# Optimization experiments

Measured on AMD Instinct MI355X. Metric: run time of the kernel, lower is better.

The kernel has to match this reference:

```python
import jax, jax.numpy as jnp
import numpy as np
import math

D_MODEL = 1024
N_HEADS = 16
HEAD_DIM = 64
BATCH = 2
SEQ = 2048


def setup_inputs() -> dict:
    key = jax.random.key(0)
    ks = jax.random.split(key, 5)
    x = jax.random.normal(ks[0], (BATCH, SEQ, D_MODEL), dtype=jnp.float32)
    s = 0.02
    wq = jax.random.normal(ks[1], (D_MODEL, D_MODEL), dtype=jnp.float32) * s
    wk = jax.random.normal(ks[2], (D_MODEL, D_MODEL), dtype=jnp.float32) * s
    wv = jax.random.normal(ks[3], (D_MODEL, D_MODEL), dtype=jnp.float32) * s
    wo = jax.random.normal(ks[4], (D_MODEL, D_MODEL), dtype=jnp.float32) * s
    gammas = jnp.linspace(0.9, 0.99, N_HEADS, dtype=jnp.float32)
    return {"x": x, "wq": wq, "wk": wk, "wv": wv, "wo": wo, "gammas": gammas}


def _decay_mask(length: int, gammas: jnp.ndarray, dtype) -> jnp.ndarray:
    # [H, L, L]: gamma^(t-s) for t >= s, else 0 (causal exponential decay)
    pos = jnp.arange(length)
    diff = pos[:, None] - pos[None, :]
    causal = diff >= 0
    d = jnp.maximum(diff, 0).astype(dtype)
    g = gammas.astype(dtype)[:, None, None]
    return jnp.where(causal[None], jnp.power(g, d[None]), jnp.zeros((), dtype))


def reference(x, wq, wk, wv, wo, gammas):
    B, L, D = x.shape
    H, hd = N_HEADS, HEAD_DIM
    # torch nn.Linear: y = x @ W.T
    q = (x @ wq.T).reshape(B, L, H, hd)
    k = (x @ wk.T).reshape(B, L, H, hd)
    v = (x @ wv.T).reshape(B, L, H, hd)
    scale = 1.0 / math.sqrt(hd)
    scores = jnp.einsum('bthd,bshd->bhts', q * scale, k)  # [B,H,L,L]
    decay = _decay_mask(L, gammas, x.dtype)               # [H,L,L]
    weights = scores * decay[None]
    retained = jnp.einsum('bhts,bshd->bthd', weights, v)  # [B,L,H,hd]
    return retained.reshape(B, L, H * hd) @ wo.T
```

## Files before the change

kernel.cpp:

```cpp
#include <hip/hip_runtime.h>


typedef __attribute__((ext_vector_type(8))) short bf16x8;
typedef __attribute__((ext_vector_type(4))) float f32x4;
typedef __attribute__((ext_vector_type(16))) float f32x16;
typedef __attribute__((ext_vector_type(4))) unsigned short u16x4;
typedef __attribute__((ext_vector_type(8))) unsigned short u16x8;
typedef __attribute__((ext_vector_type(4))) unsigned int u32x4;

__device__ inline unsigned short f2bf(float f) {
    unsigned int u;
    __builtin_memcpy(&u, &f, 4);
    u += 0x7fffu + ((u >> 16) & 1u);
    return (unsigned short)(u >> 16);
}

__device__ inline f32x4 mfma16(bf16x8 a, bf16x8 b, f32x4 c) {
    return __builtin_amdgcn_mfma_f32_16x16x32_bf16(a, b, c, 0, 0, 0);
}
__device__ inline f32x16 mfma32(bf16x8 a, bf16x8 b, f32x16 c) {
    return __builtin_amdgcn_mfma_f32_32x32x16_bf16(a, b, c, 0, 0, 0);
}

__device__ inline void gl16(const unsigned short* g, unsigned short* l) {
    __builtin_amdgcn_global_load_lds(
        (const __attribute__((address_space(1))) unsigned int*)g,
        (__attribute__((address_space(3))) unsigned int*)l,
        16, 0, 0);
}

__device__ inline unsigned cvtpk(float lo, float hi) {
    unsigned r;
    asm("v_cvt_pk_bf16_f32 %0, %1, %2" : "=v"(r) : "v"(lo), "v"(hi));
    return r;
}

__global__ __launch_bounds__(256) void convert_bf16(
    const float* __restrict__ x,
    const float* __restrict__ wq, const float* __restrict__ wk,
    const float* __restrict__ wv, const float* __restrict__ wo,
    unsigned short* __restrict__ xb,
    unsigned short* __restrict__ wqb, unsigned short* __restrict__ wkb,
    unsigned short* __restrict__ wvb, unsigned short* __restrict__ wob)
{
    int cid = blockIdx.x * 256 + threadIdx.x;
    #pragma unroll
    for (int it = 0; it < 4; ++it, cid += 262144) {
        const float* src;
        unsigned short* dst;
        size_t off;
        if (cid < 524288) {
            src = x; dst = xb; off = (size_t)cid * 8;
        } else {
            const int t = cid - 524288;
            const int seg = t >> 17;
            off = (size_t)(t & 131071) * 8;
            src = seg == 0 ? wq : seg == 1 ? wk : seg == 2 ? wv : wo;
            dst = seg == 0 ? wqb : seg == 1 ? wkb : seg == 2 ? wvb : wob;
        }
        f32x4 a = *(const f32x4*)(src + off);
        f32x4 b = *(const f32x4*)(src + off + 4);
        u32x4 v = { cvtpk(a[0], a[1]), cvtpk(a[2], a[3]),
                    cvtpk(b[0], b[1]), cvtpk(b[2], b[3]) };
        *(u32x4*)(dst + off) = v;
    }
}

__global__ __launch_bounds__(256) void qkv_bf16(
    const unsigned short* __restrict__ xb,
    const unsigned short* __restrict__ wqb, const unsigned short* __restrict__ wkb,
    const unsigned short* __restrict__ wvb,
    unsigned short* __restrict__ qfr, unsigned short* __restrict__ kfr,
    unsigned short* __restrict__ vfr)
{
    __shared__ unsigned short sR[128 * 64];
    __shared__ unsigned short sL[128 * 64];

    const int z = blockIdx.z;
    const unsigned short* W = (z == 0) ? wqb : (z == 1) ? wkb : wvb;
    const unsigned short* Rs = (z < 2) ? xb : W;
    const unsigned short* Ls = (z < 2) ? W : xb;
    const int rblk = (z < 2) ? blockIdx.x : blockIdx.y;
    const int lblk = (z < 2) ? blockIdx.y : blockIdx.x;

    const int tid = threadIdx.x;
    const int l = tid & 63, w = tid >> 6;
    const int lrow = l & 15, koff4 = (l >> 4) * 4;
    const int swz = lrow & 7;
    const int wrow = (w >> 1) * 64, wcol = (w & 1) * 64;

    f32x4 acc[4][4] = {};

    const int srow = w * 32 + (l >> 3);
    const int scol = ((l & 7) ^ ((l >> 3) & 7)) * 8;
    const unsigned short* gR = Rs + (size_t)(rblk * 128 + srow) * 1024 + scol;
    const unsigned short* gL = Ls + (size_t)(lblk * 128 + srow) * 1024 + scol;
    unsigned short* lRb = sR + (w * 32) * 64;
    unsigned short* lLb = sL + (w * 32) * 64;

    auto stage = [&](int kk) {
        #pragma unroll
        for (int p = 0; p < 4; ++p) {
            gl16(gR + (size_t)p * 8 * 1024 + kk, lRb + p * 512);
            gl16(gL + (size_t)p * 8 * 1024 + kk, lLb + p * 512);
        }
    };

    stage(0);
    for (int kk = 0; kk < 1024; kk += 64) {
        asm volatile("s_waitcnt vmcnt(0)" ::: "memory");
        __builtin_amdgcn_s_barrier();
        __builtin_amdgcn_sched_barrier(0);

        bf16x8 aL[2][4], bR[2][4];
        #pragma unroll
        for (int kt = 0; kt < 2; ++kt)
            #pragma unroll
            for (int f = 0; f < 4; ++f) {
                const int co = ((kt * 4 + (l >> 4)) ^ swz) * 8;
                aL[kt][f] = *(const bf16x8*)&sL[(wcol + f * 16 + lrow) * 64 + co];
                bR[kt][f] = *(const bf16x8*)&sR[(wrow + f * 16 + lrow) * 64 + co];
            }
        asm volatile("s_waitcnt lgkmcnt(0)" ::: "memory");
        __builtin_amdgcn_sched_barrier(0);
        __builtin_amdgcn_s_barrier();
        __builtin_amdgcn_sched_barrier(0);

        if (kk + 64 < 1024) stage(kk + 64);

        __builtin_amdgcn_s_setprio(1);
        #pragma unroll
        for (int kt = 0; kt < 2; ++kt)
            #pragma unroll
            for (int af = 0; af < 4; ++af)
                #pragma unroll
                for (int bf = 0; bf < 4; ++bf)
                    acc[af][bf] = mfma16(aL[kt][af], bR[kt][bf], acc[af][bf]);
        __builtin_amdgcn_s_setprio(0);
    }

    #pragma unroll
    for (int af = 0; af < 4; ++af) {
        #pragma unroll
        for (int bf = 0; bf < 4; ++bf) {
            const int m = rblk * 128 + wrow + bf * 16 + lrow;
            const int n0 = lblk * 128 + wcol + af * 16 + koff4;
            f32x4 v = acc[af][bf];
            unsigned p0 = cvtpk(v[0], v[1]), p1 = cvtpk(v[2], v[3]);
            u16x4 val = { (unsigned short)(p0 & 0xffff), (unsigned short)(p0 >> 16),
                          (unsigned short)(p1 & 0xffff), (unsigned short)(p1 >> 16) };
            if (z < 2) {
                const int bq = m >> 11, s = m & 2047;
                const int h2 = n0 >> 6, dd = n0 & 63;
                const size_t addr = (size_t)((bq * 16 + h2) * 64 + (s >> 5)) * 2048
                                  + (size_t)(dd >> 4) * 512 + (size_t)((dd >> 3) & 1) * 256
                                  + (size_t)(s & 31) * 8 + (dd & 7);
                unsigned short* dst = z ? kfr : qfr;
                *(u16x4*)(dst + addr) = val;
            } else {
                const int h2 = m >> 6, dd = m & 63;
                const int bq = n0 >> 11, t = n0 & 2047;
                const size_t addr = (size_t)((bq * 16 + h2) * 64 + (t >> 5)) * 2048
                                  + (size_t)((dd >> 5) * 2 + ((t >> 4) & 1)) * 512
                                  + (size_t)((t >> 3) & 1) * 256
                                  + (size_t)(dd & 31) * 8 + (t & 7);
                *(u16x4*)(vfr + addr) = val;
            }
        }
    }
}

__global__ __launch_bounds__(256) void retention_shared(
    const unsigned short* __restrict__ qfr, const unsigned short* __restrict__ kfr,
    const unsigned short* __restrict__ vfr, const float* __restrict__ gammas,
    unsigned short* __restrict__ ret)
{
    __shared__ unsigned short kv[2][4096];

    const int bid = blockIdx.x;
    const int xcd = bid & 7;
    const int j = bid >> 3;
    const int m = j & 3;
    const int pp = 15 - (j >> 2);
    const int b = m >> 1;
    const int pi = b ? (7 - xcd) : xcd;
    const int h = (m & 1) ? (15 - pi) : pi;
    const float lg = log2f(gammas[h]);
    const int cut_i = (int)(45.0f / (-lg));

    const int tid = threadIdx.x;
    const int l = tid & 63, w = tid >> 6;
    const int l31 = l & 31, hi = l >> 5;
    const int tw = pp * 4 + w;
    const int twB = pp * 4 + 3;
    const int tw0 = tw << 5;
    const int tq = tw0 + l31;

    const size_t hbase = (size_t)((b * 16 + h) * 64) * 2048;
    const unsigned short* qfb = qfr + hbase + l * 8;
    const unsigned short* kfb = kfr + hbase + l * 8;
    const unsigned short* vfb = vfr + hbase + l * 8;

    bf16x8 qf[4];
    #pragma unroll
    for (int kt = 0; kt < 4; ++kt)
        qf[kt] = *(const bf16x8*)(qfb + (size_t)tw * 2048 + kt * 512);

    float cf[16];
    #pragma unroll
    for (int r = 0; r < 16; ++r) {
        const int crow = (r & 3) + (hi << 2) + ((r >> 2) << 3);
        cf[r] = exp2f((float)(31 - crow) * lg);
    }

    int lo = ((pp * 4) << 5) - 31 - cut_i;
    lo = (lo <= 0) ? 0 : (lo >> 5);

    auto stage = [&](int sb, int bufi) {
        const unsigned short* kp = kfb + (size_t)sb * 2048 + w * 512;
        const unsigned short* vp = vfb + (size_t)sb * 2048 + w * 512;
        unsigned short* s = &kv[bufi][0];
        gl16(kp, s + w * 512);
        gl16(vp, s + 2048 + w * 512);
    };

    f32x16 acc0 = {}, acc1 = {};

    stage(lo, 0);
    if (lo + 1 <= twB) stage(lo + 1, 1);

    for (int sb = lo; sb <= twB; ++sb) {
        const int cur = (sb - lo) & 1;
        if (sb < twB) asm volatile("s_waitcnt vmcnt(2)" ::: "memory");
        else          asm volatile("s_waitcnt vmcnt(0)" ::: "memory");
        __builtin_amdgcn_sched_barrier(0);
        __builtin_amdgcn_s_barrier();
        __builtin_amdgcn_sched_barrier(0);

        bf16x8 kc[4], vc[4];
        const unsigned short* kvc = &kv[cur][0];
        #pragma unroll
        for (int kt = 0; kt < 4; ++kt)
            kc[kt] = *(const bf16x8*)(kvc + kt * 512 + l * 8);
        #pragma unroll
        for (int i = 0; i < 4; ++i)
            vc[i] = *(const bf16x8*)(kvc + 2048 + i * 512 + l * 8);
        asm volatile("s_waitcnt lgkmcnt(0)" ::: "memory");
        __builtin_amdgcn_sched_barrier(0);
        __builtin_amdgcn_s_barrier();
        __builtin_amdgcn_sched_barrier(0);

        if (sb + 2 <= twB) stage(sb + 2, cur);

        if (sb <= tw) {
            f32x16 sc = {};
            __builtin_amdgcn_s_setprio(1);
            #pragma unroll
            for (int kt = 0; kt < 4; ++kt) sc = mfma32(kc[kt], qf[kt], sc);
            __builtin_amdgcn_s_setprio(0);

            const float rowf = 0.125f * exp2f((float)(tq - (sb << 5) - 31) * lg);
            float wv_[16];
            if (sb == tw) {
                #pragma unroll
                for (int r = 0; r < 16; ++r) {
                    const int crow = (r & 3) + (hi << 2) + ((r >> 2) << 3);
                    float t_ = sc[r] * rowf * cf[r];
                    wv_[r] = (l31 >= crow) ? t_ : 0.0f;
                }
            } else {
                #pragma unroll
                for (int r = 0; r < 16; ++r)
                    wv_[r] = sc[r] * rowf * cf[r];
            }
            unsigned pk_[8];
            #pragma unroll
            for (int i = 0; i < 8; ++i) pk_[i] = cvtpk(wv_[2 * i], wv_[2 * i + 1]);
            asm("v_permlane32_swap_b32 %0, %1" : "+v"(pk_[0]), "+v"(pk_[2]));
            asm("v_permlane32_swap_b32 %0, %1" : "+v"(pk_[1]), "+v"(pk_[3]));
            asm("v_permlane32_swap_b32 %0, %1" : "+v"(pk_[4]), "+v"(pk_[6]));
            asm("v_permlane32_swap_b32 %0, %1" : "+v"(pk_[5]), "+v"(pk_[7]));
            u32x4 f0v = { pk_[0], pk_[1], pk_[2], pk_[3] };
            u32x4 f1v = { pk_[4], pk_[5], pk_[6], pk_[7] };
            const bf16x8 pa0 = __builtin_bit_cast(bf16x8, f0v);
            const bf16x8 pa1 = __builtin_bit_cast(bf16x8, f1v);
            __builtin_amdgcn_s_setprio(1);
            acc0 = mfma32(pa0, vc[0], acc0);
            acc0 = mfma32(pa1, vc[1], acc0);
            acc1 = mfma32(pa0, vc[2], acc1);
            acc1 = mfma32(pa1, vc[3], acc1);
            __builtin_amdgcn_s_setprio(0);
        }
    }

    #pragma unroll
    for (int r = 0; r < 16; ++r) {
        const int tl = (r & 3) + (hi << 2) + ((r >> 2) << 3);
        unsigned short* dst = ret + (size_t)(b * 2048 + tw0 + tl) * 1024 + h * 64 + l31;
        dst[0]  = f2bf(acc0[r]);
        dst[32] = f2bf(acc1[r]);
    }
}

__global__ __launch_bounds__(256) void out_bf16(
    const unsigned short* __restrict__ ret, const unsigned short* __restrict__ wob,
    float* __restrict__ out)
{
    __shared__ unsigned short sR[128 * 64];
    __shared__ unsigned short sL[128 * 64];

    const int rblk = blockIdx.x;
    const int lblk = blockIdx.y;

    const int tid = threadIdx.x;
    const int l = tid & 63, w = tid >> 6;
    const int lrow = l & 15, koff4 = (l >> 4) * 4;
    const int swz = lrow & 7;
    const int wrow = (w >> 1) * 64, wcol = (w & 1) * 64;

    f32x4 acc[4][4] = {};

    const int srow = w * 32 + (l >> 3);
    const int scol = ((l & 7) ^ ((l >> 3) & 7)) * 8;
    const unsigned short* gR = ret + (size_t)(rblk * 128 + srow) * 1024 + scol;
    const unsigned short* gL = wob + (size_t)(lblk * 128 + srow) * 1024 + scol;
    unsigned short* lRb = sR + (w * 32) * 64;
    unsigned short* lLb = sL + (w * 32) * 64;

    auto stage = [&](int kk) {
        #pragma unroll
        for (int p = 0; p < 4; ++p) {
            gl16(gR + (size_t)p * 8 * 1024 + kk, lRb + p * 512);
            gl16(gL + (size_t)p * 8 * 1024 + kk, lLb + p * 512);
        }
    };

    stage(0);
    for (int kk = 0; kk < 1024; kk += 64) {
        asm volatile("s_waitcnt vmcnt(0)" ::: "memory");
        __builtin_amdgcn_s_barrier();
        __builtin_amdgcn_sched_barrier(0);

        bf16x8 aL[2][4], bR[2][4];
        #pragma unroll
        for (int kt = 0; kt < 2; ++kt)
            #pragma unroll
            for (int f = 0; f < 4; ++f) {
                const int co = ((kt * 4 + (l >> 4)) ^ swz) * 8;
                aL[kt][f] = *(const bf16x8*)&sL[(wcol + f * 16 + lrow) * 64 + co];
                bR[kt][f] = *(const bf16x8*)&sR[(wrow + f * 16 + lrow) * 64 + co];
            }
        asm volatile("s_waitcnt lgkmcnt(0)" ::: "memory");
        __builtin_amdgcn_sched_barrier(0);
        __builtin_amdgcn_s_barrier();
        __builtin_amdgcn_sched_barrier(0);

        if (kk + 64 < 1024) stage(kk + 64);

        __builtin_amdgcn_s_setprio(1);
        #pragma unroll
        for (int kt = 0; kt < 2; ++kt)
            #pragma unroll
            for (int af = 0; af < 4; ++af)
                #pragma unroll
                for (int bf = 0; bf < 4; ++bf)
                    acc[af][bf] = mfma16(aL[kt][af], bR[kt][bf], acc[af][bf]);
        __builtin_amdgcn_s_setprio(0);
    }

    #pragma unroll
    for (int af = 0; af < 4; ++af)
        #pragma unroll
        for (int bf = 0; bf < 4; ++bf) {
            const int m = rblk * 128 + wrow + bf * 16 + lrow;
            const int n0 = lblk * 128 + wcol + af * 16 + koff4;
            *(f32x4*)(out + (size_t)m * 1024 + n0) = acc[af][bf];
        }
}

extern "C" void kernel_launch(void* const* d_in, const int* in_sizes, int n_in,
                              void* d_out, int out_size, void* d_ws, size_t ws_size,
                              hipStream_t stream) {
    const float* x      = (const float*)d_in[0];
    const float* wq     = (const float*)d_in[1];
    const float* wk     = (const float*)d_in[2];
    const float* wv     = (const float*)d_in[3];
    const float* wo     = (const float*)d_in[4];
    const float* gammas = (const float*)d_in[5];
    float* out = (float*)d_out;

    unsigned short* ws = (unsigned short*)d_ws;
    unsigned short* qf  = ws;
    unsigned short* kf  = ws + (size_t)4 * 1024 * 1024;
    unsigned short* vf  = ws + (size_t)8 * 1024 * 1024;
    unsigned short* ret = ws + (size_t)12 * 1024 * 1024;
    unsigned short* xb  = ret;
    unsigned short* wqb = ws + (size_t)16 * 1024 * 1024;
    unsigned short* wkb = ws + (size_t)17 * 1024 * 1024;
    unsigned short* wvb = ws + (size_t)18 * 1024 * 1024;
    unsigned short* wob = ws + (size_t)19 * 1024 * 1024;

    convert_bf16<<<1024, 256, 0, stream>>>(x, wq, wk, wv, wo, xb, wqb, wkb, wvb, wob);
    qkv_bf16<<<dim3(32, 8, 3), 256, 0, stream>>>(xb, wqb, wkb, wvb, qf, kf, vf);
    retention_shared<<<512, 256, 0, stream>>>(qf, kf, vf, gammas, ret);
    out_bf16<<<dim3(32, 8), 256, 0, stream>>>(ret, wob, out);
}
```

Baseline: 96.21 us.

## Replace windowed quadratic retention with chunkwise recurrent state formulation

Replaces the single quadratic retention kernel, which covered a decay-truncated window, with a chunkwise scheme. A local kernel handles intra-chunk attention over 64-token chunks and emits per-chunk KV states. A sequential scan then accumulates the states with gamma^64 decay, and an apply kernel adds the inter-chunk contribution q·S. The QKV kernel also writes a decay-scaled transposed K copy. This drops the long windowed loops for heads with gamma near 1, but adds two launches, a 32-step serial scan over only 32 blocks, and a bf16 read-modify-write of ret that adds rounding.

```diff
diff --git a/kernel.cpp b/kernel.cpp
--- a/kernel.cpp
+++ b/kernel.cpp
@@ -13,6 +13,12 @@
     __builtin_memcpy(&u, &f, 4);
     u += 0x7fffu + ((u >> 16) & 1u);
     return (unsigned short)(u >> 16);
+}
+__device__ inline float bf2f(unsigned short us) {
+    unsigned int u = (unsigned int)us << 16;
+    float f;
+    __builtin_memcpy(&f, &u, 4);
+    return f;
 }
 
 __device__ inline f32x4 mfma16(bf16x8 a, bf16x8 b, f32x4 c) {
@@ -69,9 +75,9 @@
 __global__ __launch_bounds__(256) void qkv_bf16(
     const unsigned short* __restrict__ xb,
     const unsigned short* __restrict__ wqb, const unsigned short* __restrict__ wkb,
-    const unsigned short* __restrict__ wvb,
+    const unsigned short* __restrict__ wvb, const float* __restrict__ gammas,
     unsigned short* __restrict__ qfr, unsigned short* __restrict__ kfr,
-    unsigned short* __restrict__ vfr)
+    unsigned short* __restrict__ vfr, unsigned short* __restrict__ kftr)
 {
     __shared__ unsigned short sR[128 * 64];
     __shared__ unsigned short sL[128 * 64];
@@ -157,6 +163,19 @@
                                   + (size_t)(s & 31) * 8 + (dd & 7);
                 unsigned short* dst = z ? kfr : qfr;
                 *(u16x4*)(dst + addr) = val;
+                if (z == 1) {
+                    const float lgh = log2f(gammas[h2 & 15]);
+                    const float fac = exp2f(lgh * (float)(64 - (s & 63)));
+                    const size_t kb2 = (size_t)((bq * 16 + h2) * 64 + (s >> 5)) * 2048
+                                     + (size_t)((s >> 4) & 1) * 512
+                                     + (size_t)((s >> 3) & 1) * 256 + (s & 7);
+                    #pragma unroll
+                    for (int q4 = 0; q4 < 4; ++q4) {
+                        const int dk = dd + q4;
+                        kftr[kb2 + (size_t)(dk >> 5) * 1024 + (size_t)(dk & 31) * 8] =
+                            f2bf(v[q4] * fac);
+                    }
+                }
             } else {
                 const int h2 = m >> 6, dd = m & 63;
                 const int bq = n0 >> 11, t = n0 & 2047;
@@ -170,41 +189,33 @@
     }
 }
 
-__global__ __launch_bounds__(256) void retention_shared(
+__global__ __launch_bounds__(128) void chunk_local(
     const unsigned short* __restrict__ qfr, const unsigned short* __restrict__ kfr,
-    const unsigned short* __restrict__ vfr, const float* __restrict__ gammas,
-    unsigned short* __restrict__ ret)
+    const unsigned short* __restrict__ vfr, const unsigned short* __restrict__ kft,
+    const float* __restrict__ gammas, unsigned short* __restrict__ ret,
+    unsigned short* __restrict__ states)
 {
-    __shared__ unsigned short kv[2][4096];
-
     const int bid = blockIdx.x;
-    const int xcd = bid & 7;
-    const int j = bid >> 3;
-    const int m = j & 3;
-    const int pp = 15 - (j >> 2);
-    const int b = m >> 1;
-    const int pi = b ? (7 - xcd) : xcd;
-    const int h = (m & 1) ? (15 - pi) : pi;
+    const int bh = bid & 31, c = bid >> 5;
+    const int b = bh >> 4, h = bh & 15;
     const float lg = log2f(gammas[h]);
-    const int cut_i = (int)(45.0f / (-lg));
 
     const int tid = threadIdx.x;
     const int l = tid & 63, w = tid >> 6;
     const int l31 = l & 31, hi = l >> 5;
-    const int tw = pp * 4 + w;
-    const int twB = pp * 4 + 3;
-    const int tw0 = tw << 5;
-    const int tq = tw0 + l31;
 
     const size_t hbase = (size_t)((b * 16 + h) * 64) * 2048;
     const unsigned short* qfb = qfr + hbase + l * 8;
     const unsigned short* kfb = kfr + hbase + l * 8;
     const unsigned short* vfb = vfr + hbase + l * 8;
+    const unsigned short* ktb = kft + hbase + l * 8;
+
+    const int gt = 2 * c + w;
 
     bf16x8 qf[4];
     #pragma unroll
     for (int kt = 0; kt < 4; ++kt)
-        qf[kt] = *(const bf16x8*)(qfb + (size_t)tw * 2048 + kt * 512);
+        qf[kt] = *(const bf16x8*)(qfb + (size_t)gt * 2048 + kt * 512);
 
     float cf[16];
     #pragma unroll
@@ -213,92 +224,170 @@
         cf[r] = exp2f((float)(31 - crow) * lg);
     }
 
-    int lo = ((pp * 4) << 5) - 31 - cut_i;
-    lo = (lo <= 0) ? 0 : (lo >> 5);
-
-    auto stage = [&](int sb, int bufi) {
-        const unsigned short* kp = kfb + (size_t)sb * 2048 + w * 512;
-        const unsigned short* vp = vfb + (size_t)sb * 2048 + w * 512;
-        unsigned short* s = &kv[bufi][0];
-        gl16(kp, s + w * 512);
-        gl16(vp, s + 2048 + w * 512);
-    };
-
     f32x16 acc0 = {}, acc1 = {};
-
-    stage(lo, 0);
-    if (lo + 1 <= twB) stage(lo + 1, 1);
-
-    for (int sb = lo; sb <= twB; ++sb) {
-        const int cur = (sb - lo) & 1;
-        if (sb < twB) asm volatile("s_waitcnt vmcnt(2)" ::: "memory");
-        else          asm volatile("s_waitcnt vmcnt(0)" ::: "memory");
-        __builtin_amdgcn_sched_barrier(0);
-        __builtin_amdgcn_s_barrier();
-        __builtin_amdgcn_sched_barrier(0);
-
+    for (int sl = 0; sl <= w; ++sl) {
+        const int gs = 2 * c + sl;
         bf16x8 kc[4], vc[4];
-        const unsigned short* kvc = &kv[cur][0];
         #pragma unroll
         for (int kt = 0; kt < 4; ++kt)
-            kc[kt] = *(const bf16x8*)(kvc + kt * 512 + l * 8);
+            kc[kt] = *(const bf16x8*)(kfb + (size_t)gs * 2048 + kt * 512);
         #pragma unroll
         for (int i = 0; i < 4; ++i)
-            vc[i] = *(const bf16x8*)(kvc + 2048 + i * 512 + l * 8);
-        asm volatile("s_waitcnt lgkmcnt(0)" ::: "memory");
-        __builtin_amdgcn_sched_barrier(0);
-        __builtin_amdgcn_s_barrier();
-        __builtin_amdgcn_sched_barrier(0);
-
-        if (sb + 2 <= twB) stage(sb + 2, cur);
-
-        if (sb <= tw) {
-            f32x16 sc = {};
-            __builtin_amdgcn_s_setprio(1);
+            vc[i] = *(const bf16x8*)(vfb + (size_t)gs * 2048 + i * 512);
+
+        f32x16 sc = {};
+        #pragma unroll
+        for (int kt = 0; kt < 4; ++kt) sc = mfma32(kc[kt], qf[kt], sc);
+
+        const float rowf = 0.125f * exp2f((float)((w - sl) * 32 + l31 - 31) * lg);
+        float wv_[16];
+        if (sl == w) {
             #pragma unroll
-            for (int kt = 0; kt < 4; ++kt) sc = mfma32(kc[kt], qf[kt], sc);
-            __builtin_amdgcn_s_setprio(0);
-
-            const float rowf = 0.125f * exp2f((float)(tq - (sb << 5) - 31) * lg);
-            float wv_[16];
-            if (sb == tw) {
-                #pragma unroll
-                for (int r = 0; r < 16; ++r) {
-                    const int crow = (r & 3) + (hi << 2) + ((r >> 2) << 3);
-                    float t_ = sc[r] * rowf * cf[r];
-                    wv_[r] = (l31 >= crow) ? t_ : 0.0f;
-                }
-            } else {
-                #pragma unroll
-                for (int r = 0; r < 16; ++r)
-                    wv_[r] = sc[r] * rowf * cf[r];
+            for (int r = 0; r < 16; ++r) {
+                const int crow = (r & 3) + (hi << 2) + ((r >> 2) << 3);
+                float t_ = sc[r] * rowf * cf[r];
+                wv_[r] = (l31 >= crow) ? t_ : 0.0f;
             }
-            unsigned pk_[8];
+        } else {
             #pragma unroll
-            for (int i = 0; i < 8; ++i) pk_[i] = cvtpk(wv_[2 * i], wv_[2 * i + 1]);
-            asm("v_permlane32_swap_b32 %0, %1" : "+v"(pk_[0]), "+v"(pk_[2]));
-            asm("v_permlane32_swap_b32 %0, %1" : "+v"(pk_[1]), "+v"(pk_[3]));
-            asm("v_permlane32_swap_b32 %0, %1" : "+v"(pk_[4]), "+v"(pk_[6]));
-            asm("v_permlane32_swap_b32 %0, %1" : "+v"(pk_[5]), "+v"(pk_[7]));
-            u32x4 f0v = { pk_[0], pk_[1], pk_[2], pk_[3] };
-            u32x4 f1v = { pk_[4], pk_[5], pk_[6], pk_[7] };
-            const bf16x8 pa0 = __builtin_bit_cast(bf16x8, f0v);
-            const bf16x8 pa1 = __builtin_bit_cast(bf16x8, f1v);
-            __builtin_amdgcn_s_setprio(1);
-            acc0 = mfma32(pa0, vc[0], acc0);
-            acc0 = mfma32(pa1, vc[1], acc0);
-            acc1 = mfma32(pa0, vc[2], acc1);
-            acc1 = mfma32(pa1, vc[3], acc1);
-            __builtin_amdgcn_s_setprio(0);
-        }
-    }
-
+            for (int r = 0; r < 16; ++r) wv_[r] = sc[r] * rowf * cf[r];
+        }
+        unsigned pk_[8];
+        #pragma unroll
+        for (int i = 0; i < 8; ++i) pk_[i] = cvtpk(wv_[2 * i], wv_[2 * i + 1]);
+        asm("v_permlane32_swap_b32 %0, %1" : "+v"(pk_[0]), "+v"(pk_[2]));
+        asm("v_permlane32_swap_b32 %0, %1" : "+v"(pk_[1]), "+v"(pk_[3]));
+        asm("v_permlane32_swap_b32 %0, %1" : "+v"(pk_[4]), "+v"(pk_[6]));
+        asm("v_permlane32_swap_b32 %0, %1" : "+v"(pk_[5]), "+v"(pk_[7]));
+        u32x4 f0v = { pk_[0], pk_[1], pk_[2], pk_[3] };
+        u32x4 f1v = { pk_[4], pk_[5], pk_[6], pk_[7] };
+        const bf16x8 pa0 = __builtin_bit_cast(bf16x8, f0v);
+        const bf16x8 pa1 = __builtin_bit_cast(bf16x8, f1v);
+        acc0 = mfma32(pa0, vc[0], acc0);
+        acc0 = mfma32(pa1, vc[1], acc0);
+        acc1 = mfma32(pa0, vc[2], acc1);
+        acc1 = mfma32(pa1, vc[3], acc1);
+    }
     #pragma unroll
     for (int r = 0; r < 16; ++r) {
         const int tl = (r & 3) + (hi << 2) + ((r >> 2) << 3);
-        unsigned short* dst = ret + (size_t)(b * 2048 + tw0 + tl) * 1024 + h * 64 + l31;
+        unsigned short* dst = ret + (size_t)(b * 2048 + gt * 32 + tl) * 1024 + h * 64 + l31;
         dst[0]  = f2bf(acc0[r]);
         dst[32] = f2bf(acc1[r]);
+    }
+
+    f32x16 as0 = {}, as1 = {};
+    #pragma unroll
+    for (int sl = 0; sl < 2; ++sl) {
+        const int gs = 2 * c + sl;
+        bf16x8 vc[4];
+        #pragma unroll
+        for (int i = 0; i < 4; ++i)
+            vc[i] = *(const bf16x8*)(vfb + (size_t)gs * 2048 + i * 512);
+        bf16x8 kt0 = *(const bf16x8*)(ktb + (size_t)gs * 2048 + (w * 2 + 0) * 512);
+        bf16x8 kt1 = *(const bf16x8*)(ktb + (size_t)gs * 2048 + (w * 2 + 1) * 512);
+        as0 = mfma32(kt0, vc[0], as0);
+        as0 = mfma32(kt1, vc[1], as0);
+        as1 = mfma32(kt0, vc[2], as1);
+        as1 = mfma32(kt1, vc[3], as1);
+    }
+    unsigned short* sbase = states + (size_t)(bh * 32 + c) * 4096;
+    #pragma unroll
+    for (int r = 0; r < 16; ++r) {
+        const int crow = (r & 3) + (hi << 2) + ((r >> 2) << 3);
+        const size_t a = (size_t)(2 * w + (crow >> 4)) * 1024
+                       + (size_t)((crow >> 3) & 1) * 256 + (crow & 7) + (size_t)l31 * 8;
+        sbase[a]       = f2bf(as0[r]);
+        sbase[a + 512] = f2bf(as1[r]);
+    }
+}
+
+__global__ __launch_bounds__(256) void state_scan(
+    unsigned short* __restrict__ states, const float* __restrict__ gammas)
+{
+    const int bh = blockIdx.x;
+    const float g64 = exp2f(64.0f * log2f(gammas[bh & 15]));
+    unsigned short* base = states + (size_t)bh * 32 * 4096 + threadIdx.x * 16;
+
+    float S[16] = {};
+    u16x8 a0 = *(const u16x8*)(base);
+    u16x8 a1 = *(const u16x8*)(base + 8);
+    for (int c = 0; c < 32; ++c) {
+        u16x8 n0, n1;
+        if (c + 1 < 32) {
+            n0 = *(const u16x8*)(base + (size_t)(c + 1) * 4096);
+            n1 = *(const u16x8*)(base + (size_t)(c + 1) * 4096 + 8);
+        }
+        u16x8 o0, o1;
+        #pragma unroll
+        for (int e = 0; e < 8; ++e) {
+            S[e] = S[e] * g64 + bf2f(a0[e]);
+            o0[e] = f2bf(S[e]);
+        }
+        #pragma unroll
+        for (int e = 0; e < 8; ++e) {
+            S[8 + e] = S[8 + e] * g64 + bf2f(a1[e]);
+            o1[e] = f2bf(S[8 + e]);
+        }
+        *(u16x8*)(base + (size_t)c * 4096) = o0;
+        *(u16x8*)(base + (size_t)c * 4096 + 8) = o1;
+        a0 = n0; a1 = n1;
+    }
+}
+
+__global__ __launch_bounds__(64) void inter_apply(
+    const unsigned short* __restrict__ qfr, const unsigned short* __restrict__ states,
+    const float* __restrict__ gammas, unsigned short* __restrict__ ret)
+{
+    const int bid = blockIdx.x;
+    const int bh = bid & 31;
+    const int c = 1 + (bid >> 5);
+    const int b = bh >> 4, h = bh & 15;
+    const float lg = log2f(gammas[h]);
+
+    const int l = threadIdx.x, l31 = l & 31, hi = l >> 5;
+
+    const unsigned short* sb_ = states + (size_t)(bh * 32 + c - 1) * 4096 + l * 8;
+    bf16x8 sf[4][2];
+    #pragma unroll
+    for (int kt = 0; kt < 4; ++kt)
+        #pragma unroll
+        for (int dh = 0; dh < 2; ++dh)
+            sf[kt][dh] = *(const bf16x8*)(sb_ + kt * 1024 + dh * 512);
+
+    const size_t hbase = (size_t)((b * 16 + h) * 64) * 2048;
+    const unsigned short* qfb = qfr + hbase + l * 8;
+
+    float cfac[16];
+    #pragma unroll
+    for (int r = 0; r < 16; ++r) {
+        const int crow = (r & 3) + (hi << 2) + ((r >> 2) << 3);
+        cfac[r] = 0.125f * exp2f((float)crow * lg);
+    }
+    const float g32 = exp2f(32.0f * lg);
+
+    #pragma unroll
+    for (int ti = 0; ti < 2; ++ti) {
+        const int gt = 2 * c + ti;
+        bf16x8 qf[4];
+        #pragma unroll
+        for (int kt = 0; kt < 4; ++kt)
+            qf[kt] = *(const bf16x8*)(qfb + (size_t)gt * 2048 + kt * 512);
+        f32x16 a0 = {}, a1 = {};
+        #pragma unroll
+        for (int kt = 0; kt < 4; ++kt) {
+            a0 = mfma32(qf[kt], sf[kt][0], a0);
+            a1 = mfma32(qf[kt], sf[kt][1], a1);
+        }
+        const float tf = ti ? g32 : 1.0f;
+        #pragma unroll
+        for (int r = 0; r < 16; ++r) {
+            const int tl = (r & 3) + (hi << 2) + ((r >> 2) << 3);
+            const float sfac = cfac[r] * tf;
+            unsigned short* dst = ret + (size_t)(b * 2048 + gt * 32 + tl) * 1024 + h * 64 + l31;
+            dst[0]  = f2bf(bf2f(dst[0])  + a0[r] * sfac);
+            dst[32] = f2bf(bf2f(dst[32]) + a1[r] * sfac);
+        }
     }
 }
 
@@ -390,18 +479,24 @@
     float* out = (float*)d_out;
 
     unsigned short* ws = (unsigned short*)d_ws;
-    unsigned short* qf  = ws;
-    unsigned short* kf  = ws + (size_t)4 * 1024 * 1024;
-    unsigned short* vf  = ws + (size_t)8 * 1024 * 1024;
-    unsigned short* ret = ws + (size_t)12 * 1024 * 1024;
-    unsigned short* xb  = ret;
-    unsigned short* wqb = ws + (size_t)16 * 1024 * 1024;
-    unsigned short* wkb = ws + (size_t)17 * 1024 * 1024;
-    unsigned short* wvb = ws + (size_t)18 * 1024 * 1024;
-    unsigned short* wob = ws + (size_t)19 * 1024 * 1024;
+    const size_t M = 1024 * 1024;
+    unsigned short* qf     = ws;
+    unsigned short* kf     = ws + 4 * M;
+    unsigned short* vf     = ws + 8 * M;
+    unsigned short* ret    = ws + 12 * M;
+    unsigned short* xb     = ret;
+    unsigned short* wqb    = ws + 16 * M;
+    unsigned short* wkb    = ws + 17 * M;
+    unsigned short* wvb    = ws + 18 * M;
+    unsigned short* states = ws + 16 * M;
+    unsigned short* kft    = ws + 20 * M;
+    unsigned short* wob    = ws + 24 * M;
 
     convert_bf16<<<1024, 256, 0, stream>>>(x, wq, wk, wv, wo, xb, wqb, wkb, wvb, wob);
-    qkv_bf16<<<dim3(32, 8, 3), 256, 0, stream>>>(xb, wqb, wkb, wvb, qf, kf, vf);
-    retention_shared<<<512, 256, 0, stream>>>(qf, kf, vf, gammas, ret);
+    qkv_bf16<<<dim3(32, 8, 3), 256, 0, stream>>>(xb, wqb, wkb, wvb, gammas,
+                                                 qf, kf, vf, kft);
+    chunk_local<<<1024, 128, 0, stream>>>(qf, kf, vf, kft, gammas, ret, states);
+    state_scan<<<32, 256, 0, stream>>>(states, gammas);
+    inter_apply<<<992, 64, 0, stream>>>(qf, states, gammas, ret);
     out_bf16<<<dim3(32, 8), 256, 0, stream>>>(ret, wob, out);
 }
```

Result: no change. 95.89 us (-0.3%).
